# Kernel optimization log

Hardware: AMD Instinct MI355X
Metric: run time of the kernel (lower is better)

## Reference

```python
import jax, jax.numpy as jnp
import numpy as np

DIM = 64
HID = 64
BATCH = 16384
L = DIM - 1  # number of FCNN layers (for dims 1..DIM-1)


def setup_inputs() -> dict:
    key = jax.random.key(0)
    ks = jax.random.split(key, 8)
    bound = float(np.sqrt(0.5))
    return {
        "x": jax.random.normal(ks[0], (BATCH, DIM), jnp.float32),
        "initial_param": jax.random.uniform(ks[1], (2,), jnp.float32, -bound, bound),
        # padded per-layer weights: layer l uses input columns 0..l only (masked in reference)
        "W1": jax.random.normal(ks[2], (L, L, HID), jnp.float32) * 0.1,
        "b1": jnp.zeros((L, HID), jnp.float32),
        "W2": jax.random.normal(ks[3], (L, HID, HID), jnp.float32) * 0.1,
        "b2": jnp.zeros((L, HID), jnp.float32),
        "W3": jax.random.normal(ks[4], (L, HID, 2), jnp.float32) * 0.1,
        "b3": jnp.zeros((L, 2), jnp.float32),
    }


def reference(x, initial_param, W1, b1, W2, b2, W3, b3):
    B = x.shape[0]
    # mask[l, j] = 1 if input column j is visible to layer l (layer l == FCNN(in_dim=l+1))
    mask = (jnp.arange(L)[None, :] <= jnp.arange(L)[:, None]).astype(x.dtype)  # [L, L]
    xin = x[:, :L]                                                             # [B, L]
    # all per-dim FCNNs in one batched pass (equivalent to the Python loop over x[:, :i])
    h1 = jnp.tanh(jnp.einsum('bj,ljh->blh', xin, W1 * mask[:, :, None]) + b1)  # [B, L, H]
    h2 = jnp.tanh(jnp.einsum('blh,lhk->blk', h1, W2) + b2)                     # [B, L, H]
    out = jnp.einsum('blh,lhk->blk', h2, W3) + b3                              # [B, L, 2]
    mu0 = jnp.full((B, 1), initial_param[0], x.dtype)
    a0 = jnp.full((B, 1), initial_param[1], x.dtype)
    mu = jnp.concatenate([mu0, out[..., 0]], axis=1)      # [B, DIM]
    alpha = jnp.concatenate([a0, out[..., 1]], axis=1)    # [B, DIM]
    z = (x - mu) * jnp.exp(-alpha)
    log_det = -jnp.sum(alpha, axis=1)                     # [B]
    return z[:, ::-1], log_det
```

## Files before the change

kernel.cpp:

```cpp
#include <hip/hip_runtime.h>

#define LN 63
#define BATCHN 16384

typedef __attribute__((ext_vector_type(8))) short bf16x8;
typedef __attribute__((ext_vector_type(4))) float f32x4;

__device__ __forceinline__ float fast_exp(float v) {
    return __builtin_amdgcn_exp2f(v * 1.4426950408889634f);
}
__device__ __forceinline__ float fast_tanh(float v) {
    float e = __builtin_amdgcn_exp2f(v * 2.8853900817779268f);
    return 1.0f - 2.0f * __builtin_amdgcn_rcpf(e + 1.0f);
}
__device__ __forceinline__ short f2bf(float f) {
    __bf16 h = (__bf16)f;
    return __builtin_bit_cast(short, h);
}
__device__ __forceinline__ unsigned int pk2(float a, float b) {
    return (unsigned int)(unsigned short)f2bf(a) |
           ((unsigned int)(unsigned short)f2bf(b) << 16);
}

__device__ __forceinline__ int kappa_j(int s, int g, int e) {
    return (e < 4) ? (32 * s + 4 * g + e) : (32 * s + 16 + 4 * g + e - 4);
}

__global__ __launch_bounds__(256) void prep_kernel(
    const float* __restrict__ x,
    const float* __restrict__ W1, const float* __restrict__ b1,
    const float* __restrict__ W2, const float* __restrict__ W3,
    unsigned short* __restrict__ Afrag,
    unsigned short* __restrict__ xbf)
{
    const int t = threadIdx.x;
    const int b = blockIdx.x;
    if (b >= LN) {
        const int i = ((b - LN) * 256 + t) * 4;
        const float4 v = *reinterpret_cast<const float4*>(x + i);
        ushort4 o;
        o.x = (unsigned short)f2bf(v.x);
        o.y = (unsigned short)f2bf(v.y);
        o.z = (unsigned short)f2bf(v.z);
        o.w = (unsigned short)f2bf(v.w);
        *reinterpret_cast<ushort4*>(xbf + i) = o;
        return;
    }
    const int l = b;
    unsigned short* Af = Afrag + (size_t)l * 9216;

    #pragma unroll
    for (int it = 0; it < 2; ++it) {
        const int item = t + it * 256;
        const int s = item >> 8, tt = (item >> 6) & 3, lane = item & 63;
        const int g = lane >> 4, mcol = lane & 15, h = 16 * tt + mcol;
        unsigned pk[4];
        #pragma unroll
        for (int ep = 0; ep < 4; ++ep) {
            float v[2];
            #pragma unroll
            for (int k = 0; k < 2; ++k) {
                const int e = 2 * ep + k;
                const int j = 32 * s + 8 * g + e;
                float val;
                if (j == 63)      val = b1[l * 64 + h];
                else if (j <= l)  val = W1[(l * LN + j) * 64 + h];
                else              val = 0.0f;
                v[k] = val;
            }
            pk[ep] = pk2(v[0], v[1]);
        }
        *reinterpret_cast<uint4*>(Af + ((size_t)item) * 8) =
            uint4{pk[0], pk[1], pk[2], pk[3]};
    }
    #pragma unroll
    for (int it = 0; it < 2; ++it) {
        const int item = t + it * 256;
        const int s = item >> 8, tt = (item >> 6) & 3, lane = item & 63;
        const int g = lane >> 4, mcol = lane & 15, h = 16 * tt + mcol;
        unsigned pk[4];
        #pragma unroll
        for (int ep = 0; ep < 4; ++ep) {
            float v[2];
            #pragma unroll
            for (int k = 0; k < 2; ++k) {
                const int e = 2 * ep + k;
                v[k] = W2[(l * 64 + kappa_j(s, g, e)) * 64 + h];
            }
            pk[ep] = pk2(v[0], v[1]);
        }
        *reinterpret_cast<uint4*>(Af + 4096 + ((size_t)item) * 8) =
            uint4{pk[0], pk[1], pk[2], pk[3]};
    }
    if (t < 128) {
        const int s = t >> 6, lane = t & 63;
        const int g = lane >> 4, mcol = lane & 15;
        unsigned pk[4] = {0u, 0u, 0u, 0u};
        if (mcol < 2) {
            #pragma unroll
            for (int ep = 0; ep < 4; ++ep) {
                float v[2];
                #pragma unroll
                for (int k = 0; k < 2; ++k) {
                    const int e = 2 * ep + k;
                    v[k] = W3[(l * 64 + kappa_j(s, g, e)) * 2 + mcol];
                }
                pk[ep] = pk2(v[0], v[1]);
            }
        }
        *reinterpret_cast<uint4*>(Af + 8192 + ((size_t)t) * 8) =
            uint4{pk[0], pk[1], pk[2], pk[3]};
    }
}

template<int XBF>
__global__ __launch_bounds__(256, 2) void maf_main_kernel(
    const float* __restrict__ x,
    const unsigned short* __restrict__ xbf,
    const unsigned short* __restrict__ Afrag,
    const float* __restrict__ b2,
    const float* __restrict__ b3,
    float* __restrict__ zT,
    float* __restrict__ aT)
{
    const int t = threadIdx.x;
    const int bid = blockIdx.x;
    const int l = bid % LN;
    const int rowBase = (bid / LN) * 1024;

    const int lane = t & 63;
    const int w = t >> 6;
    const int g = lane >> 4;
    const int mcol = lane & 15;

    const unsigned short* Af = Afrag + (size_t)l * 9216;
    bf16x8 w1f[2][4], w2f[2][4], w3f[2];
    #pragma unroll
    for (int s = 0; s < 2; ++s) {
        #pragma unroll
        for (int tt = 0; tt < 4; ++tt) {
            w1f[s][tt] = *reinterpret_cast<const bf16x8*>(Af + ((s * 4 + tt) * 64 + lane) * 8);
            w2f[s][tt] = *reinterpret_cast<const bf16x8*>(Af + 4096 + ((s * 4 + tt) * 64 + lane) * 8);
        }
        w3f[s] = *reinterpret_cast<const bf16x8*>(Af + 8192 + (s * 64 + lane) * 8);
    }
    f32x4 bias2[4];
    #pragma unroll
    for (int tt = 0; tt < 4; ++tt) {
        const float4 v2 = *reinterpret_cast<const float4*>(&b2[l * 64 + 16 * tt + 4 * g]);
        bias2[tt] = f32x4{v2.x, v2.y, v2.z, v2.w};
    }
    const float b30 = b3[l * 2 + 0];
    const float b31 = b3[l * 2 + 1];
    const short one_bf = (short)0x3F80;

    #pragma unroll 2
    for (int grp = 0; grp < 16; ++grp) {
        const int row = rowBase + w * 256 + grp * 16 + mcol;

        bf16x8 xf[2];
        if constexpr (XBF) {
            xf[0] = *reinterpret_cast<const bf16x8*>(xbf + (size_t)row * 64 + 8 * g);
            xf[1] = *reinterpret_cast<const bf16x8*>(xbf + (size_t)row * 64 + 32 + 8 * g);
        } else {
            const float* xr = x + (size_t)row * 64;
            #pragma unroll
            for (int s = 0; s < 2; ++s) {
                const float4 a = *reinterpret_cast<const float4*>(xr + 32 * s + 8 * g);
                const float4 b = *reinterpret_cast<const float4*>(xr + 32 * s + 8 * g + 4);
                bf16x8 f;
                f[0] = f2bf(a.x); f[1] = f2bf(a.y); f[2] = f2bf(a.z); f[3] = f2bf(a.w);
                f[4] = f2bf(b.x); f[5] = f2bf(b.y); f[6] = f2bf(b.z); f[7] = f2bf(b.w);
                xf[s] = f;
            }
        }
        if (g == 3) xf[1][7] = one_bf;

        f32x4 c1[4];
        #pragma unroll
        for (int tt = 0; tt < 4; ++tt) c1[tt] = f32x4{0.0f, 0.0f, 0.0f, 0.0f};
        #pragma unroll
        for (int s = 0; s < 2; ++s)
            #pragma unroll
            for (int tt = 0; tt < 4; ++tt)
                c1[tt] = __builtin_amdgcn_mfma_f32_16x16x32_bf16(w1f[s][tt], xf[s], c1[tt], 0, 0, 0);

        bf16x8 pf[2];
        #pragma unroll
        for (int s = 0; s < 2; ++s) {
            bf16x8 f;
            #pragma unroll
            for (int q = 0; q < 4; ++q) {
                f[q]     = f2bf(fast_tanh(c1[2 * s][q]));
                f[4 + q] = f2bf(fast_tanh(c1[2 * s + 1][q]));
            }
            pf[s] = f;
        }

        f32x4 c2[4];
        #pragma unroll
        for (int tt = 0; tt < 4; ++tt) c2[tt] = bias2[tt];
        #pragma unroll
        for (int s = 0; s < 2; ++s)
            #pragma unroll
            for (int tt = 0; tt < 4; ++tt)
                c2[tt] = __builtin_amdgcn_mfma_f32_16x16x32_bf16(w2f[s][tt], pf[s], c2[tt], 0, 0, 0);

        bf16x8 qf[2];
        #pragma unroll
        for (int s = 0; s < 2; ++s) {
            bf16x8 f;
            #pragma unroll
            for (int q = 0; q < 4; ++q) {
                f[q]     = f2bf(fast_tanh(c2[2 * s][q]));
                f[4 + q] = f2bf(fast_tanh(c2[2 * s + 1][q]));
            }
            qf[s] = f;
        }

        f32x4 c3 = {0.0f, 0.0f, 0.0f, 0.0f};
        c3 = __builtin_amdgcn_mfma_f32_16x16x32_bf16(w3f[0], qf[0], c3, 0, 0, 0);
        c3 = __builtin_amdgcn_mfma_f32_16x16x32_bf16(w3f[1], qf[1], c3, 0, 0, 0);

        if (g == 0) {
            const float mu = c3[0] + b30;
            const float al = c3[1] + b31;
            const float xn = x[(size_t)row * 64 + l + 1];
            const float zv = (xn - mu) * fast_exp(-al);
            zT[(62 - l) * BATCHN + row] = zv;
            aT[l * BATCHN + row] = al;
        }
    }
}

__global__ __launch_bounds__(256) void maf_finish_kernel(
    const float* __restrict__ x,
    const float* __restrict__ ip,
    const float* __restrict__ zT,
    const float* __restrict__ aT,
    float* __restrict__ z_out,
    float* __restrict__ ld_out)
{
    __shared__ float tile[64][65];

    const int t = threadIdx.x;
    const int rb = blockIdx.x * 64;
    const float mu0 = ip[0];
    const float a0  = ip[1];
    const float e0  = fast_exp(-a0);

    {
        const int r = t >> 2, c = t & 3;
        const int row = rb + r;
        float s = 0.0f;
        for (int i = c; i < LN; i += 4) s += aT[(size_t)i * BATCHN + row];
        s += __shfl_xor(s, 1, 64);
        s += __shfl_xor(s, 2, 64);
        if (c == 0) ld_out[row] = -(s + a0);
    }

    const int r = t & 63, cq = t >> 6;
    #pragma unroll
    for (int k = 0; k < 16; ++k) {
        const int c = cq * 16 + k;
        float v;
        if (c < 63) v = zT[(size_t)c * BATCHN + rb + r];
        else        v = (x[(size_t)(rb + r) * 64] - mu0) * e0;
        tile[c][r] = v;
    }
    __syncthreads();
    #pragma unroll
    for (int i = 0; i < 16; ++i) {
        const int rr = cq * 16 + i;
        z_out[(size_t)(rb + rr) * 64 + r] = tile[r][rr];
    }
}

extern "C" void kernel_launch(void* const* d_in, const int* in_sizes, int n_in,
                              void* d_out, int out_size, void* d_ws, size_t ws_size,
                              hipStream_t stream) {
    const float* x  = (const float*)d_in[0];
    const float* ip = (const float*)d_in[1];
    const float* W1 = (const float*)d_in[2];
    const float* b1 = (const float*)d_in[3];
    const float* W2 = (const float*)d_in[4];
    const float* b2 = (const float*)d_in[5];
    const float* W3 = (const float*)d_in[6];
    const float* b3 = (const float*)d_in[7];

    float* z_out  = (float*)d_out;
    float* ld_out = z_out + (size_t)BATCHN * 64;

    unsigned short* Afrag = (unsigned short*)d_ws;
    float* zT = (float*)((char*)d_ws + (size_t)LN * 9216 * 2);
    float* aT = zT + (size_t)LN * BATCHN;
    unsigned short* xbf = (unsigned short*)(aT + (size_t)LN * BATCHN);

    const size_t need_xbf = (size_t)LN * 9216 * 2 + (size_t)LN * BATCHN * 8 +
                            (size_t)BATCHN * 64 * 2;
    if (ws_size >= need_xbf) {
        prep_kernel<<<dim3(LN + BATCHN * 64 / 1024), dim3(256), 0, stream>>>(
            x, W1, b1, W2, W3, Afrag, xbf);
        maf_main_kernel<1><<<dim3(LN * 16), dim3(256), 0, stream>>>(
            x, xbf, Afrag, b2, b3, zT, aT);
    } else {
        prep_kernel<<<dim3(LN), dim3(256), 0, stream>>>(
            x, W1, b1, W2, W3, Afrag, xbf);
        maf_main_kernel<0><<<dim3(LN * 16), dim3(256), 0, stream>>>(
            x, xbf, Afrag, b2, b3, zT, aT);
    }
    maf_finish_kernel<<<dim3(BATCHN / 64), dim3(256), 0, stream>>>(
        x, ip, zT, aT, z_out, ld_out);
}
```

Baseline: 66.16 us.

## Interleave two row groups per iteration and prefetch next x fragments

The main loop now processes two 16-row groups per iteration with independent MFMA chains interleaved, and software-prefetches the next pair of bf16 x fragments into registers. W1 fragments are reloaded inside the loop instead of being held for the whole kernel, which frees registers for the doubled accumulators. The fallback path without bf16 x is dropped, so the code now assumes the workspace is large enough. The aim is to hide MFMA and tanh latency and global load latency, at the cost of higher register pressure and repeated W1 loads.

New measurement: 65.62 us. No clear change (-0.8%).

```diff
diff --git a/kernel.cpp b/kernel.cpp
--- a/kernel.cpp
+++ b/kernel.cpp
@@ -113,6 +113,8 @@
     }
 }
 
+struct ChainOut { float mu, al; };
+
 template<int XBF>
 __global__ __launch_bounds__(256, 2) void maf_main_kernel(
     const float* __restrict__ x,
@@ -134,14 +136,12 @@
     const int mcol = lane & 15;
 
     const unsigned short* Af = Afrag + (size_t)l * 9216;
-    bf16x8 w1f[2][4], w2f[2][4], w3f[2];
+    bf16x8 w2f[2][4], w3f[2];
     #pragma unroll
     for (int s = 0; s < 2; ++s) {
         #pragma unroll
-        for (int tt = 0; tt < 4; ++tt) {
-            w1f[s][tt] = *reinterpret_cast<const bf16x8*>(Af + ((s * 4 + tt) * 64 + lane) * 8);
+        for (int tt = 0; tt < 4; ++tt)
             w2f[s][tt] = *reinterpret_cast<const bf16x8*>(Af + 4096 + ((s * 4 + tt) * 64 + lane) * 8);
-        }
         w3f[s] = *reinterpret_cast<const bf16x8*>(Af + 8192 + (s * 64 + lane) * 8);
     }
     f32x4 bias2[4];
@@ -154,82 +154,112 @@
     const float b31 = b3[l * 2 + 1];
     const short one_bf = (short)0x3F80;
 
-    #pragma unroll 2
-    for (int grp = 0; grp < 16; ++grp) {
-        const int row = rowBase + w * 256 + grp * 16 + mcol;
-
-        bf16x8 xf[2];
-        if constexpr (XBF) {
-            xf[0] = *reinterpret_cast<const bf16x8*>(xbf + (size_t)row * 64 + 8 * g);
-            xf[1] = *reinterpret_cast<const bf16x8*>(xbf + (size_t)row * 64 + 32 + 8 * g);
-        } else {
-            const float* xr = x + (size_t)row * 64;
-            #pragma unroll
-            for (int s = 0; s < 2; ++s) {
-                const float4 a = *reinterpret_cast<const float4*>(xr + 32 * s + 8 * g);
-                const float4 b = *reinterpret_cast<const float4*>(xr + 32 * s + 8 * g + 4);
-                bf16x8 f;
-                f[0] = f2bf(a.x); f[1] = f2bf(a.y); f[2] = f2bf(a.z); f[3] = f2bf(a.w);
-                f[4] = f2bf(b.x); f[5] = f2bf(b.y); f[6] = f2bf(b.z); f[7] = f2bf(b.w);
-                xf[s] = f;
-            }
-        }
-        if (g == 3) xf[1][7] = one_bf;
-
-        f32x4 c1[4];
-        #pragma unroll
-        for (int tt = 0; tt < 4; ++tt) c1[tt] = f32x4{0.0f, 0.0f, 0.0f, 0.0f};
+    const int rowW = rowBase + w * 256 + mcol;
+    const unsigned short* xrow = xbf + (size_t)rowW * 64 + 8 * g;
+
+    auto ldxf = [&](int k, bf16x8& f0, bf16x8& f1) {
+        const unsigned short* p = xrow + (size_t)(16 * k) * 64;
+        f0 = *reinterpret_cast<const bf16x8*>(p);
+        f1 = *reinterpret_cast<const bf16x8*>(p + 32);
+        if (g == 3) f1[7] = one_bf;
+    };
+
+    bf16x8 xa0, xa1, xb0, xb1, na0, na1, nb0, nb1;
+    ldxf(0, xa0, xa1);
+    ldxf(1, xb0, xb1);
+
+    #pragma unroll 1
+    for (int it = 0; it < 8; ++it) {
+        const int nk = (it < 7) ? (2 * it + 2) : 14;
+        ldxf(nk, na0, na1);
+        ldxf(nk + 1, nb0, nb1);
+
+        bf16x8 w1f[2][4];
         #pragma unroll
         for (int s = 0; s < 2; ++s)
             #pragma unroll
             for (int tt = 0; tt < 4; ++tt)
-                c1[tt] = __builtin_amdgcn_mfma_f32_16x16x32_bf16(w1f[s][tt], xf[s], c1[tt], 0, 0, 0);
-
-        bf16x8 pf[2];
+                w1f[s][tt] = *reinterpret_cast<const bf16x8*>(Af + ((s * 4 + tt) * 64 + lane) * 8);
+
+        f32x4 c1a[4], c1b[4];
+        #pragma unroll
+        for (int tt = 0; tt < 4; ++tt) {
+            c1a[tt] = f32x4{0.0f, 0.0f, 0.0f, 0.0f};
+            c1b[tt] = f32x4{0.0f, 0.0f, 0.0f, 0.0f};
+        }
+        #pragma unroll
+        for (int tt = 0; tt < 4; ++tt) {
+            c1a[tt] = __builtin_amdgcn_mfma_f32_16x16x32_bf16(w1f[0][tt], xa0, c1a[tt], 0, 0, 0);
+            c1b[tt] = __builtin_amdgcn_mfma_f32_16x16x32_bf16(w1f[0][tt], xb0, c1b[tt], 0, 0, 0);
+        }
+        #pragma unroll
+        for (int tt = 0; tt < 4; ++tt) {
+            c1a[tt] = __builtin_amdgcn_mfma_f32_16x16x32_bf16(w1f[1][tt], xa1, c1a[tt], 0, 0, 0);
+            c1b[tt] = __builtin_amdgcn_mfma_f32_16x16x32_bf16(w1f[1][tt], xb1, c1b[tt], 0, 0, 0);
+        }
+
+        bf16x8 pfa[2], pfb[2];
         #pragma unroll
         for (int s = 0; s < 2; ++s) {
-            bf16x8 f;
+            bf16x8 fa, fb;
             #pragma unroll
             for (int q = 0; q < 4; ++q) {
-                f[q]     = f2bf(fast_tanh(c1[2 * s][q]));
-                f[4 + q] = f2bf(fast_tanh(c1[2 * s + 1][q]));
-            }
-            pf[s] = f;
-        }
-
-        f32x4 c2[4];
-        #pragma unroll
-        for (int tt = 0; tt < 4; ++tt) c2[tt] = bias2[tt];
+                fa[q]     = f2bf(fast_tanh(c1a[2 * s][q]));
+                fb[q]     = f2bf(fast_tanh(c1b[2 * s][q]));
+                fa[4 + q] = f2bf(fast_tanh(c1a[2 * s + 1][q]));
+                fb[4 + q] = f2bf(fast_tanh(c1b[2 * s + 1][q]));
+            }
+            pfa[s] = fa;
+            pfb[s] = fb;
+        }
+
+        f32x4 c2a[4], c2b[4];
+        #pragma unroll
+        for (int tt = 0; tt < 4; ++tt) { c2a[tt] = bias2[tt]; c2b[tt] = bias2[tt]; }
         #pragma unroll
         for (int s = 0; s < 2; ++s)
             #pragma unroll
-            for (int tt = 0; tt < 4; ++tt)
-                c2[tt] = __builtin_amdgcn_mfma_f32_16x16x32_bf16(w2f[s][tt], pf[s], c2[tt], 0, 0, 0);
-
-        bf16x8 qf[2];
+            for (int tt = 0; tt < 4; ++tt) {
+                c2a[tt] = __builtin_amdgcn_mfma_f32_16x16x32_bf16(w2f[s][tt], pfa[s], c2a[tt], 0, 0, 0);
+                c2b[tt] = __builtin_amdgcn_mfma_f32_16x16x32_bf16(w2f[s][tt], pfb[s], c2b[tt], 0, 0, 0);
+            }
+
+        bf16x8 qfa[2], qfb[2];
         #pragma unroll
         for (int s = 0; s < 2; ++s) {
-            bf16x8 f;
+            bf16x8 fa, fb;
             #pragma unroll
             for (int q = 0; q < 4; ++q) {
-                f[q]     = f2bf(fast_tanh(c2[2 * s][q]));
-                f[4 + q] = f2bf(fast_tanh(c2[2 * s + 1][q]));
-            }
-            qf[s] = f;
-        }
-
-        f32x4 c3 = {0.0f, 0.0f, 0.0f, 0.0f};
-        c3 = __builtin_amdgcn_mfma_f32_16x16x32_bf16(w3f[0], qf[0], c3, 0, 0, 0);
-        c3 = __builtin_amdgcn_mfma_f32_16x16x32_bf16(w3f[1], qf[1], c3, 0, 0, 0);
+                fa[q]     = f2bf(fast_tanh(c2a[2 * s][q]));
+                fb[q]     = f2bf(fast_tanh(c2b[2 * s][q]));
+                fa[4 + q] = f2bf(fast_tanh(c2a[2 * s + 1][q]));
+                fb[4 + q] = f2bf(fast_tanh(c2b[2 * s + 1][q]));
+            }
+            qfa[s] = fa;
+            qfb[s] = fb;
+        }
+
+        f32x4 c3a = {0.0f, 0.0f, 0.0f, 0.0f};
+        f32x4 c3b = {0.0f, 0.0f, 0.0f, 0.0f};
+        c3a = __builtin_amdgcn_mfma_f32_16x16x32_bf16(w3f[0], qfa[0], c3a, 0, 0, 0);
+        c3b = __builtin_amdgcn_mfma_f32_16x16x32_bf16(w3f[0], qfb[0], c3b, 0, 0, 0);
+        c3a = __builtin_amdgcn_mfma_f32_16x16x32_bf16(w3f[1], qfa[1], c3a, 0, 0, 0);
+        c3b = __builtin_amdgcn_mfma_f32_16x16x32_bf16(w3f[1], qfb[1], c3b, 0, 0, 0);
 
         if (g == 0) {
-            const float mu = c3[0] + b30;
-            const float al = c3[1] + b31;
-            const float xn = x[(size_t)row * 64 + l + 1];
-            const float zv = (xn - mu) * fast_exp(-al);
-            zT[(62 - l) * BATCHN + row] = zv;
-            aT[l * BATCHN + row] = al;
-        }
+            const int rowA = rowW + 32 * it;
+            const int rowB = rowA + 16;
+            const float muA = c3a[0] + b30, alA = c3a[1] + b31;
+            const float muB = c3b[0] + b30, alB = c3b[1] + b31;
+            const float xnA = x[(size_t)rowA * 64 + l + 1];
+            const float xnB = x[(size_t)rowB * 64 + l + 1];
+            zT[(62 - l) * BATCHN + rowA] = (xnA - muA) * fast_exp(-alA);
+            zT[(62 - l) * BATCHN + rowB] = (xnB - muB) * fast_exp(-alB);
+            aT[l * BATCHN + rowA] = alA;
+            aT[l * BATCHN + rowB] = alB;
+        }
+
+        xa0 = na0; xa1 = na1; xb0 = nb0; xb1 = nb1;
     }
 }
 
@@ -296,19 +326,10 @@
     float* aT = zT + (size_t)LN * BATCHN;
     unsigned short* xbf = (unsigned short*)(aT + (size_t)LN * BATCHN);
 
-    const size_t need_xbf = (size_t)LN * 9216 * 2 + (size_t)LN * BATCHN * 8 +
-                            (size_t)BATCHN * 64 * 2;
-    if (ws_size >= need_xbf) {
-        prep_kernel<<<dim3(LN + BATCHN * 64 / 1024), dim3(256), 0, stream>>>(
-            x, W1, b1, W2, W3, Afrag, xbf);
-        maf_main_kernel<1><<<dim3(LN * 16), dim3(256), 0, stream>>>(
-            x, xbf, Afrag, b2, b3, zT, aT);
-    } else {
-        prep_kernel<<<dim3(LN), dim3(256), 0, stream>>>(
-            x, W1, b1, W2, W3, Afrag, xbf);
-        maf_main_kernel<0><<<dim3(LN * 16), dim3(256), 0, stream>>>(
-            x, xbf, Afrag, b2, b3, zT, aT);
-    }
+    prep_kernel<<<dim3(LN + BATCHN * 64 / 1024), dim3(256), 0, stream>>>(
+        x, W1, b1, W2, W3, Afrag, xbf);
+    maf_main_kernel<1><<<dim3(LN * 16), dim3(256), 0, stream>>>(
+        x, xbf, Afrag, b2, b3, zT, aT);
     maf_finish_kernel<<<dim3(BATCHN / 64), dim3(256), 0, stream>>>(
         x, ip, zT, aT, z_out, ld_out);
 }
```
